# Kernel tuning notes

Measured on AMD Instinct MI355X. Metric: run time of the kernel, lower is better.

The kernel has to match this reference:

```python
import jax, jax.numpy as jnp
import numpy as np

B = 4096      # batch
D = 256       # flattened input feature dim
NUMFEAT = 1 + D + D * (D + 1) // 2  # 33153: bias + linear + quadratic terms


def setup_inputs() -> dict:
    key = jax.random.key(0)
    k1, k2 = jax.random.split(key)
    x = jax.random.normal(k1, (B, D), dtype=jnp.float32)
    # nn.Linear(numfeat, 10, bias=False): weight shape (10, numfeat)
    W = jax.random.normal(k2, (10, NUMFEAT), dtype=jnp.float32) * 0.01
    return {"x": x, "W": W}


def reference(x, W):
    # x: (B, D) -- original does x.view(B, -1); already 2D here.
    b, d = x.shape
    # sklearn PolynomialFeatures(degree=2) column order:
    # [1, x_0..x_{d-1}, x_0*x_0, x_0*x_1, ..., x_{d-1}*x_{d-1}]
    # i.e. combinations_with_replacement == upper-triangular (incl. diagonal)
    iu0, iu1 = np.triu_indices(d)  # static index constants
    ones = jnp.ones((b, 1), dtype=x.dtype)
    cross = x[:, iu0] * x[:, iu1]          # (B, D*(D+1)/2)
    feats = jnp.concatenate([ones, x, cross], axis=1)  # (B, NUMFEAT)
    return feats @ W.T                      # (B, 10)
```

## Files before the change

kernel.cpp:

```cpp
#include <hip/hip_runtime.h>


#define DD 256
#define NF 33153
#define TPB 256
#define MROWS 64
#define ASTRIDE 264

typedef __attribute__((ext_vector_type(8))) short short8;
typedef __attribute__((ext_vector_type(4))) float floatx4;
typedef __attribute__((ext_vector_type(4), aligned(4))) float float4a;

union S8U { unsigned u[4]; short8 s; };

__device__ inline unsigned pack2(float lo, float hi) {
    unsigned a = __builtin_bit_cast(unsigned, hi) + 0x8000u;
    unsigned b = __builtin_bit_cast(unsigned, lo) + 0x8000u;
    return __builtin_amdgcn_perm(a, b, 0x07060302u);
}

__device__ inline short8 load_pack8(const float* __restrict__ p) {
    float4a v0 = *(const float4a*)p;
    float4a v1 = *(const float4a*)(p + 4);
    S8U r;
    r.u[0] = pack2(v0.x, v0.y); r.u[1] = pack2(v0.z, v0.w);
    r.u[2] = pack2(v1.x, v1.y); r.u[3] = pack2(v1.z, v1.w);
    return r.s;
}

__device__ inline int troff(int i) { return 257 + 255 * i - ((i * (i - 1)) >> 1); }

__global__ __launch_bounds__(TPB, 3)
void PolynomialRegression_75385265979710_kernel(const float* __restrict__ x,
                                                const float* __restrict__ W,
                                                float* __restrict__ out) {
    __shared__ __align__(16) unsigned short As[MROWS * ASTRIDE];
    __shared__ float red[4 * MROWS];

    const int tid  = threadIdx.x;
    const int lane = tid & 63, wave = tid >> 6;
    const int ln   = lane & 15, quad = lane >> 4;
    const int q8   = quad * 8;
    const int rowbase = blockIdx.x * MROWS;
    const int o0 = blockIdx.y * 2;
    const int g1 = wave, g2 = 7 - wave;
    const int rem = 8 - wave;

#pragma unroll
    for (int it = 0; it < 8; ++it) {
        int idx = it * 2048 + tid * 8;
        int r = idx >> 8, c = idx & 255;
        const float* src = &x[(rowbase + r) * DD + c];
        float4a v0 = *(const float4a*)src;
        float4a v1 = *(const float4a*)(src + 4);
        S8U p;
        p.u[0] = pack2(v0.x, v0.y); p.u[1] = pack2(v0.z, v0.w);
        p.u[2] = pack2(v1.x, v1.y); p.u[3] = pack2(v1.z, v1.w);
        *(short8*)&As[r * ASTRIDE + c] = p.s;
    }

    const int offA0 = troff(g1 * 32 + ln)      + q8;
    const int offA1 = troff(g1 * 32 + 16 + ln) + q8;
    const int offB0 = troff(g2 * 32 + ln)      + q8;
    const int offB1 = troff(g2 * 32 + 16 + ln) + q8;

    unsigned mA[4], mB[4];
#pragma unroll
    for (int w2 = 0; w2 < 4; ++w2) {
        mA[w2] = ((q8 + 2 * w2     < ln) ? 0u : 0x0000FFFFu)
               | ((q8 + 2 * w2 + 1 < ln) ? 0u : 0xFFFF0000u);
        mB[w2] = ((q8 + 2 * w2     < 16 + ln) ? 0u : 0x0000FFFFu)
               | ((q8 + 2 * w2 + 1 < 16 + ln) ? 0u : 0xFFFF0000u);
    }

    int iRow[4];
#pragma unroll
    for (int nt = 0; nt < 4; ++nt) {
        int g = (nt < 2) ? g1 : g2;
        iRow[nt] = g * 32 + (nt & 1) * 16 + ln;
    }

    S8U pb0, pb1;
    pb0.s = load_pack8(W + o0 * NF + offA0 + g1 * 32);
    pb1.s = load_pack8(W + o0 * NF + offA1 + g1 * 32);

    __syncthreads();

#pragma unroll
    for (int oo = 0; oo < 2; ++oo) {
        const int o = o0 + oo;
        const float* __restrict__ Wo = W + o * NF;

        float w1v[4];
#pragma unroll
        for (int nt = 0; nt < 4; ++nt) w1v[nt] = Wo[1 + iRow[nt]];
        const float bias = Wo[0];

        floatx4 acc[4][4];
#pragma unroll
        for (int mt = 0; mt < 4; ++mt)
#pragma unroll
            for (int nt = 0; nt < 4; ++nt) acc[mt][nt] = (floatx4)0.f;

#pragma unroll
        for (int t = 0; t < 9; ++t) {
            const bool first = (t < rem);
            const int kc = first ? (g1 + t) : (g2 + (t - rem));
            const int co = kc * 32;
            S8U b0, b1;
            if (t == 0) {
                b0 = pb0; b1 = pb1;
            } else {
                b0.s = load_pack8(Wo + (first ? offA0 : offB0) + co);
                b1.s = load_pack8(Wo + (first ? offA1 : offB1) + co);
            }
            if (t == 0 || t == rem) {
#pragma unroll
                for (int w2 = 0; w2 < 4; ++w2) { b0.u[w2] &= mA[w2]; b1.u[w2] &= mB[w2]; }
            }
            short8 a[4];
#pragma unroll
            for (int mt = 0; mt < 4; ++mt)
                a[mt] = *(const short8*)&As[(mt * 16 + ln) * ASTRIDE + co + q8];
            if (first) {
#pragma unroll
                for (int mt = 0; mt < 4; ++mt) {
                    acc[mt][0] = __builtin_amdgcn_mfma_f32_16x16x32_bf16(a[mt], b0.s, acc[mt][0], 0, 0, 0);
                    acc[mt][1] = __builtin_amdgcn_mfma_f32_16x16x32_bf16(a[mt], b1.s, acc[mt][1], 0, 0, 0);
                }
            } else {
#pragma unroll
                for (int mt = 0; mt < 4; ++mt) {
                    acc[mt][2] = __builtin_amdgcn_mfma_f32_16x16x32_bf16(a[mt], b0.s, acc[mt][2], 0, 0, 0);
                    acc[mt][3] = __builtin_amdgcn_mfma_f32_16x16x32_bf16(a[mt], b1.s, acc[mt][3], 0, 0, 0);
                }
            }
        }

        if (oo == 0) {
            pb0.s = load_pack8(W + (o0 + 1) * NF + offA0 + g1 * 32);
            pb1.s = load_pack8(W + (o0 + 1) * NF + offA1 + g1 * 32);
        }

#pragma unroll
        for (int mt = 0; mt < 4; ++mt) {
#pragma unroll
            for (int r = 0; r < 4; ++r) {
                const int m = mt * 16 + quad * 4 + r;
                float p = 0.f;
#pragma unroll
                for (int nt = 0; nt < 4; ++nt) {
                    unsigned u = As[m * ASTRIDE + iRow[nt]];
                    float xv = __builtin_bit_cast(float, u << 16);
                    p = fmaf(xv, acc[mt][nt][r] + w1v[nt], p);
                }
                p += __shfl_xor(p, 1);
                p += __shfl_xor(p, 2);
                p += __shfl_xor(p, 4);
                p += __shfl_xor(p, 8);
                if (ln == 0) red[wave * MROWS + m] = p;
            }
        }
        __syncthreads();

        if (tid < MROWS) {
            float s = bias;
#pragma unroll
            for (int w = 0; w < 4; ++w) s += red[w * MROWS + tid];
            out[(rowbase + tid) * 10 + o] = s;
        }
        __syncthreads();
    }
}

extern "C" void kernel_launch(void* const* d_in, const int* in_sizes, int n_in,
                              void* d_out, int out_size, void* d_ws, size_t ws_size,
                              hipStream_t stream) {
    const float* x = (const float*)d_in[0];
    const float* W = (const float*)d_in[1];
    float* out = (float*)d_out;

    dim3 grid(4096 / MROWS, 5);
    PolynomialRegression_75385265979710_kernel<<<grid, TPB, 0, stream>>>(x, W, out);
}
```

Baseline: 81.80 us.

## Split output channels across grid and software-pipeline W fragment loads

```diff
diff --git a/kernel.cpp b/kernel.cpp
--- a/kernel.cpp
+++ b/kernel.cpp
@@ -19,15 +19,6 @@
     return __builtin_amdgcn_perm(a, b, 0x07060302u);
 }
 
-__device__ inline short8 load_pack8(const float* __restrict__ p) {
-    float4a v0 = *(const float4a*)p;
-    float4a v1 = *(const float4a*)(p + 4);
-    S8U r;
-    r.u[0] = pack2(v0.x, v0.y); r.u[1] = pack2(v0.z, v0.w);
-    r.u[2] = pack2(v1.x, v1.y); r.u[3] = pack2(v1.z, v1.w);
-    return r.s;
-}
-
 __device__ inline int troff(int i) { return 257 + 255 * i - ((i * (i - 1)) >> 1); }
 
 __global__ __launch_bounds__(TPB, 3)
@@ -42,9 +33,21 @@
     const int ln   = lane & 15, quad = lane >> 4;
     const int q8   = quad * 8;
     const int rowbase = blockIdx.x * MROWS;
-    const int o0 = blockIdx.y * 2;
+    const int o  = blockIdx.y;
     const int g1 = wave, g2 = 7 - wave;
     const int rem = 8 - wave;
+
+    const float* __restrict__ Wo = W + o * NF;
+
+    const int offA0 = troff(g1 * 32 + ln)      + q8;
+    const int offA1 = troff(g1 * 32 + 16 + ln) + q8;
+    const int offB0 = troff(g2 * 32 + ln)      + q8;
+    const int offB1 = troff(g2 * 32 + 16 + ln) + q8;
+
+    float4a ca0 = *(const float4a*)(Wo + offA0 + g1 * 32);
+    float4a ca1 = *(const float4a*)(Wo + offA0 + g1 * 32 + 4);
+    float4a cb0 = *(const float4a*)(Wo + offA1 + g1 * 32);
+    float4a cb1 = *(const float4a*)(Wo + offA1 + g1 * 32 + 4);
 
 #pragma unroll
     for (int it = 0; it < 8; ++it) {
@@ -59,11 +62,6 @@
         *(short8*)&As[r * ASTRIDE + c] = p.s;
     }
 
-    const int offA0 = troff(g1 * 32 + ln)      + q8;
-    const int offA1 = troff(g1 * 32 + 16 + ln) + q8;
-    const int offB0 = troff(g2 * 32 + ln)      + q8;
-    const int offB1 = troff(g2 * 32 + 16 + ln) + q8;
-
     unsigned mA[4], mB[4];
 #pragma unroll
     for (int w2 = 0; w2 < 4; ++w2) {
@@ -74,102 +72,99 @@
     }
 
     int iRow[4];
+    float w1v[4];
 #pragma unroll
     for (int nt = 0; nt < 4; ++nt) {
         int g = (nt < 2) ? g1 : g2;
         iRow[nt] = g * 32 + (nt & 1) * 16 + ln;
+        w1v[nt]  = Wo[1 + iRow[nt]];
     }
-
-    S8U pb0, pb1;
-    pb0.s = load_pack8(W + o0 * NF + offA0 + g1 * 32);
-    pb1.s = load_pack8(W + o0 * NF + offA1 + g1 * 32);
+    const float bias = Wo[0];
 
     __syncthreads();
 
+    floatx4 acc[4][4];
 #pragma unroll
-    for (int oo = 0; oo < 2; ++oo) {
-        const int o = o0 + oo;
-        const float* __restrict__ Wo = W + o * NF;
+    for (int mt = 0; mt < 4; ++mt)
+#pragma unroll
+        for (int nt = 0; nt < 4; ++nt) acc[mt][nt] = (floatx4)0.f;
 
-        float w1v[4];
 #pragma unroll
-        for (int nt = 0; nt < 4; ++nt) w1v[nt] = Wo[1 + iRow[nt]];
-        const float bias = Wo[0];
+    for (int t = 0; t < 9; ++t) {
+        const bool first = (t < rem);
+        const int kc = first ? (g1 + t) : (g2 + (t - rem));
+        const int co = kc * 32;
 
-        floatx4 acc[4][4];
+        float4a na0, na1, nb0, nb1;
+        if (t < 8) {
+            const bool nf = (t + 1 < rem);
+            const int nkc = nf ? (g1 + t + 1) : (g2 + (t + 1 - rem));
+            const int nco = nkc * 32;
+            const float* p0 = Wo + (nf ? offA0 : offB0) + nco;
+            const float* p1 = Wo + (nf ? offA1 : offB1) + nco;
+            na0 = *(const float4a*)p0; na1 = *(const float4a*)(p0 + 4);
+            nb0 = *(const float4a*)p1; nb1 = *(const float4a*)(p1 + 4);
+        }
+
+        S8U b0, b1;
+        b0.u[0] = pack2(ca0.x, ca0.y); b0.u[1] = pack2(ca0.z, ca0.w);
+        b0.u[2] = pack2(ca1.x, ca1.y); b0.u[3] = pack2(ca1.z, ca1.w);
+        b1.u[0] = pack2(cb0.x, cb0.y); b1.u[1] = pack2(cb0.z, cb0.w);
+        b1.u[2] = pack2(cb1.x, cb1.y); b1.u[3] = pack2(cb1.z, cb1.w);
+
+        if (t == 0 || t == rem) {
+#pragma unroll
+            for (int w2 = 0; w2 < 4; ++w2) { b0.u[w2] &= mA[w2]; b1.u[w2] &= mB[w2]; }
+        }
+
+        short8 a[4];
 #pragma unroll
         for (int mt = 0; mt < 4; ++mt)
+            a[mt] = *(const short8*)&As[(mt * 16 + ln) * ASTRIDE + co + q8];
+
+        if (first) {
 #pragma unroll
-            for (int nt = 0; nt < 4; ++nt) acc[mt][nt] = (floatx4)0.f;
-
+            for (int mt = 0; mt < 4; ++mt) {
+                acc[mt][0] = __builtin_amdgcn_mfma_f32_16x16x32_bf16(a[mt], b0.s, acc[mt][0], 0, 0, 0);
+                acc[mt][1] = __builtin_amdgcn_mfma_f32_16x16x32_bf16(a[mt], b1.s, acc[mt][1], 0, 0, 0);
+            }
+        } else {
 #pragma unroll
-        for (int t = 0; t < 9; ++t) {
-            const bool first = (t < rem);
-            const int kc = first ? (g1 + t) : (g2 + (t - rem));
-            const int co = kc * 32;
-            S8U b0, b1;
-            if (t == 0) {
-                b0 = pb0; b1 = pb1;
-            } else {
-                b0.s = load_pack8(Wo + (first ? offA0 : offB0) + co);
-                b1.s = load_pack8(Wo + (first ? offA1 : offB1) + co);
-            }
-            if (t == 0 || t == rem) {
-#pragma unroll
-                for (int w2 = 0; w2 < 4; ++w2) { b0.u[w2] &= mA[w2]; b1.u[w2] &= mB[w2]; }
-            }
-            short8 a[4];
-#pragma unroll
-            for (int mt = 0; mt < 4; ++mt)
-                a[mt] = *(const short8*)&As[(mt * 16 + ln) * ASTRIDE + co + q8];
-            if (first) {
-#pragma unroll
-                for (int mt = 0; mt < 4; ++mt) {
-                    acc[mt][0] = __builtin_amdgcn_mfma_f32_16x16x32_bf16(a[mt], b0.s, acc[mt][0], 0, 0, 0);
-                    acc[mt][1] = __builtin_amdgcn_mfma_f32_16x16x32_bf16(a[mt], b1.s, acc[mt][1], 0, 0, 0);
-                }
-            } else {
-#pragma unroll
-                for (int mt = 0; mt < 4; ++mt) {
-                    acc[mt][2] = __builtin_amdgcn_mfma_f32_16x16x32_bf16(a[mt], b0.s, acc[mt][2], 0, 0, 0);
-                    acc[mt][3] = __builtin_amdgcn_mfma_f32_16x16x32_bf16(a[mt], b1.s, acc[mt][3], 0, 0, 0);
-                }
+            for (int mt = 0; mt < 4; ++mt) {
+                acc[mt][2] = __builtin_amdgcn_mfma_f32_16x16x32_bf16(a[mt], b0.s, acc[mt][2], 0, 0, 0);
+                acc[mt][3] = __builtin_amdgcn_mfma_f32_16x16x32_bf16(a[mt], b1.s, acc[mt][3], 0, 0, 0);
             }
         }
 
-        if (oo == 0) {
-            pb0.s = load_pack8(W + (o0 + 1) * NF + offA0 + g1 * 32);
-            pb1.s = load_pack8(W + (o0 + 1) * NF + offA1 + g1 * 32);
-        }
+        if (t < 8) { ca0 = na0; ca1 = na1; cb0 = nb0; cb1 = nb1; }
+    }
 
 #pragma unroll
-        for (int mt = 0; mt < 4; ++mt) {
+    for (int mt = 0; mt < 4; ++mt) {
 #pragma unroll
-            for (int r = 0; r < 4; ++r) {
-                const int m = mt * 16 + quad * 4 + r;
-                float p = 0.f;
+        for (int r = 0; r < 4; ++r) {
+            const int m = mt * 16 + quad * 4 + r;
+            float p = 0.f;
 #pragma unroll
-                for (int nt = 0; nt < 4; ++nt) {
-                    unsigned u = As[m * ASTRIDE + iRow[nt]];
-                    float xv = __builtin_bit_cast(float, u << 16);
-                    p = fmaf(xv, acc[mt][nt][r] + w1v[nt], p);
-                }
-                p += __shfl_xor(p, 1);
-                p += __shfl_xor(p, 2);
-                p += __shfl_xor(p, 4);
-                p += __shfl_xor(p, 8);
-                if (ln == 0) red[wave * MROWS + m] = p;
+            for (int nt = 0; nt < 4; ++nt) {
+                unsigned u = As[m * ASTRIDE + iRow[nt]];
+                float xv = __builtin_bit_cast(float, u << 16);
+                p = fmaf(xv, acc[mt][nt][r] + w1v[nt], p);
             }
+            p += __shfl_xor(p, 1);
+            p += __shfl_xor(p, 2);
+            p += __shfl_xor(p, 4);
+            p += __shfl_xor(p, 8);
+            if (ln == 0) red[wave * MROWS + m] = p;
         }
-        __syncthreads();
+    }
+    __syncthreads();
 
-        if (tid < MROWS) {
-            float s = bias;
+    if (tid < MROWS) {
+        float s = bias;
 #pragma unroll
-            for (int w = 0; w < 4; ++w) s += red[w * MROWS + tid];
-            out[(rowbase + tid) * 10 + o] = s;
-        }
-        __syncthreads();
+        for (int w = 0; w < 4; ++w) s += red[w * MROWS + tid];
+        out[(rowbase + tid) * 10 + o] = s;
     }
 }
 
@@ -180,6 +175,6 @@
     const float* W = (const float*)d_in[1];
     float* out = (float*)d_out;
 
-    dim3 grid(4096 / MROWS, 5);
+    dim3 grid(4096 / MROWS, 10);
     PolynomialRegression_75385265979710_kernel<<<grid, TPB, 0, stream>>>(x, W, out);
 }
```

Measured after the change: 70.07 us, median of 2. 14.3% less time.
